# Kernel optimization log

Measured on AMD Instinct MI355X. Metric: run time of the kernel, lower is better.

Reference implementation:

```python
import jax, jax.numpy as jnp
import numpy as np

B, H, W = 16, 352, 352
EPS = 1e-7

# Directable[TL_table[i]] for i = 0..7: (dx, dy), dx=+1 shifts right, dy=+1 shifts down
# TL_table = [lower_right, down, lower_left, right, left, upper_right, up, upper_left]
SHIFTS = [(1, 1), (0, 1), (-1, 1), (1, 0), (-1, 0), (1, -1), (0, -1), (-1, -1)]


def _shift(x, dx, dy):
    # x: [B,H,W]; zero-padded translation, equivalent to the bmm against the
    # near-identity translation matrices in the original code.
    if dx == 1:
        x = jnp.pad(x, ((0, 0), (0, 0), (1, 0)))[:, :, :-1]
    elif dx == -1:
        x = jnp.pad(x, ((0, 0), (0, 0), (0, 1)))[:, :, 1:]
    if dy == 1:
        x = jnp.pad(x, ((0, 0), (1, 0), (0, 0)))[:, :-1, :]
    elif dy == -1:
        x = jnp.pad(x, ((0, 0), (0, 1), (0, 0)))[:, 1:, :]
    return x


def _bce_sum(p, t):
    p = jnp.clip(p, EPS, 1.0 - EPS)
    return -jnp.sum(t * jnp.log(p) + (1.0 - t) * jnp.log1p(-p))


def setup_inputs() -> dict:
    key = jax.random.key(0)
    k1, k2, k3 = jax.random.split(key, 3)
    c_map = jax.random.normal(k1, (B, 8, H, W), dtype=jnp.float32)
    target = jax.random.uniform(k2, (B, 1, H, W), dtype=jnp.float32)
    con_target = jax.random.randint(k3, (B, 8, H, W), 0, 2, dtype=jnp.int32)
    return {"c_map": c_map, "target": target, "con_target": con_target}


def reference(c_map, target, con_target):
    p = jax.nn.sigmoid(c_map)                      # [B,8,H,W]
    con = con_target.astype(p.dtype)
    sum_conn = jnp.sum(con, axis=1)                # [B,H,W]
    edge = ((sum_conn < 8) & (sum_conn > 0)).astype(p.dtype)

    # Bilateral voting: shifted[:, i] = shift(p[:, 7-i], direction_i)
    shifted = jnp.stack(
        [_shift(p[:, 7 - i], *SHIFTS[i]) for i in range(8)], axis=1
    )                                              # [B,8,H,W]
    vote = p * shifted                             # [B,8,H,W]

    glo_map = jnp.max(vote, axis=1)                # [B,H,W]
    pred_mask_min = jnp.min(vote, axis=1)          # [B,H,W]
    decouple = glo_map * (1.0 - edge) + (1.0 - pred_mask_min) * edge

    de_loss = _bce_sum(decouple[:, None], target)
    conmap_l = _bce_sum(p, con)
    bimap_l = _bce_sum(vote, con)
    return 0.8 * conmap_l + de_loss + 0.2 * bimap_l
```

## Files before the change

kernel.cpp:

```cpp
#include <hip/hip_runtime.h>


#define EPSF 1e-7f

constexpr int B = 16, H = 352, W = 352;
constexpr int HW = H * W;
constexpr int N = B * HW;
constexpr int W4 = W / 4;
constexpr int HW4 = HW / 4;
constexpr int NQ = N / 4;
constexpr int NBLK = NQ / 256;

typedef float f4 __attribute__((ext_vector_type(4)));
typedef int   i4 __attribute__((ext_vector_type(4)));

__device__ __forceinline__ float rcpf(float x) { return __builtin_amdgcn_rcpf(x); }

__device__ __forceinline__ f4 sigmoid4(f4 x) {
    f4 r;
    r.x = rcpf(1.0f + __expf(-x.x));
    r.y = rcpf(1.0f + __expf(-x.y));
    r.z = rcpf(1.0f + __expf(-x.z));
    r.w = rcpf(1.0f + __expf(-x.w));
    return r;
}
__device__ __forceinline__ f4 max4(f4 a, f4 b) {
    f4 r; r.x=fmaxf(a.x,b.x); r.y=fmaxf(a.y,b.y); r.z=fmaxf(a.z,b.z); r.w=fmaxf(a.w,b.w); return r;
}
__device__ __forceinline__ f4 min4(f4 a, f4 b) {
    f4 r; r.x=fminf(a.x,b.x); r.y=fminf(a.y,b.y); r.z=fminf(a.z,b.z); r.w=fminf(a.w,b.w); return r;
}
__device__ __forceinline__ f4 sel4(i4 q, f4 a, f4 b) {
    f4 r; r.x=q.x?a.x:b.x; r.y=q.y?a.y:b.y; r.z=q.z?a.z:b.z; r.w=q.w?a.w:b.w; return r;
}
__device__ __forceinline__ f4 loadu4(const float* p) {
    f4 v; __builtin_memcpy(&v, p, sizeof(f4)); return v;
}

__device__ __forceinline__ float finish_pixel(float glo, float pmin, int sc,
                                              float t, float cp, float ba, float bb) {
    const float edge = (sc < 8 && sc > 0) ? 1.0f : 0.0f;
    float dec = glo * (1.0f - edge) + (1.0f - pmin) * edge;
    dec = fminf(fmaxf(dec, EPSF), 1.0f - EPSF);
    const float de = -(t * __logf(dec) + (1.0f - t) * __logf(1.0f - dec));
    return de - 0.8f * __logf(cp) - 0.2f * (__logf(ba) + __logf(bb));
}

__global__ __launch_bounds__(256, 4) void bicon_loss_kernel(
    const float* __restrict__ c_map,
    const float* __restrict__ target,
    const int*   __restrict__ con,
    float* __restrict__ ws)
{
    const int tid = blockIdx.x * blockDim.x + threadIdx.x;
    const int b  = tid / HW4;
    const int rq = tid - b * HW4;
    const int y  = rq / W4;
    const int xq = rq - y * W4;
    const int x0 = xq * 4;

    const float* __restrict__ cm = c_map + (size_t)b * 8 * HW + y * W + x0;
    const int*   __restrict__ cn = con   + (size_t)b * 8 * HW + y * W + x0;

    const f4 c0 = *(const f4*)(cm + 0 * HW);
    const f4 c1 = *(const f4*)(cm + 1 * HW);
    const f4 c2 = *(const f4*)(cm + 2 * HW);
    const f4 c3 = *(const f4*)(cm + 3 * HW);
    const f4 c4 = *(const f4*)(cm + 4 * HW);
    const f4 c5 = *(const f4*)(cm + 5 * HW);
    const f4 c6 = *(const f4*)(cm + 6 * HW);
    const f4 c7 = *(const f4*)(cm + 7 * HW);
    const f4 n0 = loadu4(cm + 7 * HW - 1 * W - 1);
    const f4 n1 = *(const f4*)(cm + 6 * HW - 1 * W);
    const f4 n2 = loadu4(cm + 5 * HW - 1 * W + 1);
    const f4 n3 = loadu4(cm + 4 * HW - 1);
    const f4 n4 = loadu4(cm + 3 * HW + 1);
    const f4 n5 = loadu4(cm + 2 * HW + 1 * W - 1);
    const f4 n6 = *(const f4*)(cm + 1 * HW + 1 * W);
    const f4 n7 = loadu4(cm + 0 * HW + 1 * W + 1);
    const i4 q0 = *(const i4*)(cn + 0 * HW);
    const i4 q1 = *(const i4*)(cn + 1 * HW);
    const i4 q2 = *(const i4*)(cn + 2 * HW);
    const i4 q3 = *(const i4*)(cn + 3 * HW);
    const i4 q4 = *(const i4*)(cn + 4 * HW);
    const i4 q5 = *(const i4*)(cn + 5 * HW);
    const i4 q6 = *(const i4*)(cn + 6 * HW);
    const i4 q7 = *(const i4*)(cn + 7 * HW);
    const f4 t4 = *(const f4*)(target + (size_t)b * HW + y * W + x0);

    const f4 p0 = sigmoid4(c0);
    const f4 p1 = sigmoid4(c1);
    const f4 p2 = sigmoid4(c2);
    const f4 p3 = sigmoid4(c3);
    const f4 p4 = sigmoid4(c4);
    const f4 p5 = sigmoid4(c5);
    const f4 p6 = sigmoid4(c6);
    const f4 p7 = sigmoid4(c7);

    const float lm = (xq == 0)      ? 0.0f : 1.0f;
    const float rm = (xq == W4 - 1) ? 0.0f : 1.0f;
    const float tm = (y == 0)       ? 0.0f : 1.0f;
    const float bm = (y == H - 1)   ? 0.0f : 1.0f;

    f4 conprod = {1.f,1.f,1.f,1.f};
    f4 biA     = {1.f,1.f,1.f,1.f};
    f4 biB     = {1.f,1.f,1.f,1.f};
    f4 glo     = {-1e30f,-1e30f,-1e30f,-1e30f};
    f4 pmin    = { 1e30f, 1e30f, 1e30f, 1e30f};

#define DIR(P, Q, NR, DX, RMASK, BI) {                                        \
        f4 s = sigmoid4(NR);                                                  \
        s *= (RMASK);                                                         \
        if ((DX) == 1)  s.x *= lm;                                            \
        if ((DX) == -1) s.w *= rm;                                            \
        const f4 v = (P) * s;                                                 \
        glo  = max4(glo,  v);                                                 \
        pmin = min4(pmin, v);                                                 \
        conprod *= sel4((Q), (P), 1.0f - (P));                                \
        BI *= sel4((Q), max4(v, (f4){EPSF,EPSF,EPSF,EPSF}), 1.0f - v);        \
    }
    DIR(p0, q0, n0,  1, tm, biA)
    DIR(p1, q1, n1,  0, tm, biA)
    DIR(p2, q2, n2, -1, tm, biA)
    DIR(p3, q3, n3,  1, 1.0f, biA)
    DIR(p4, q4, n4, -1, 1.0f, biB)
    DIR(p5, q5, n5,  1, bm, biB)
    DIR(p6, q6, n6,  0, bm, biB)
    DIR(p7, q7, n7, -1, bm, biB)
#undef DIR

    const i4 sc = q0 + q1 + q2 + q3 + q4 + q5 + q6 + q7;

    float part = finish_pixel(glo.x, pmin.x, sc.x, t4.x, conprod.x, biA.x, biB.x)
               + finish_pixel(glo.y, pmin.y, sc.y, t4.y, conprod.y, biA.y, biB.y)
               + finish_pixel(glo.z, pmin.z, sc.z, t4.z, conprod.z, biA.z, biB.z)
               + finish_pixel(glo.w, pmin.w, sc.w, t4.w, conprod.w, biA.w, biB.w);

    #pragma unroll
    for (int off = 32; off > 0; off >>= 1)
        part += __shfl_down(part, off, 64);

    __shared__ float wsum[4];
    const int lane = threadIdx.x & 63;
    const int wid  = threadIdx.x >> 6;
    if (lane == 0) wsum[wid] = part;
    __syncthreads();
    if (threadIdx.x == 0) {
        ws[blockIdx.x] = wsum[0] + wsum[1] + wsum[2] + wsum[3];
    }
}

__global__ __launch_bounds__(256) void reduce_partials_kernel(
    const float* __restrict__ ws, float* __restrict__ out)
{
    float s = 0.0f;
    for (int i = threadIdx.x; i < NBLK; i += 256) s += ws[i];
    #pragma unroll
    for (int off = 32; off > 0; off >>= 1)
        s += __shfl_down(s, off, 64);
    __shared__ float wsum[4];
    const int lane = threadIdx.x & 63;
    const int wid  = threadIdx.x >> 6;
    if (lane == 0) wsum[wid] = s;
    __syncthreads();
    if (threadIdx.x == 0) out[0] = wsum[0] + wsum[1] + wsum[2] + wsum[3];
}

extern "C" void kernel_launch(void* const* d_in, const int* in_sizes, int n_in,
                              void* d_out, int out_size, void* d_ws, size_t ws_size,
                              hipStream_t stream) {
    const float* c_map  = (const float*)d_in[0];
    const float* target = (const float*)d_in[1];
    const int*   con    = (const int*)d_in[2];
    float* out = (float*)d_out;
    float* ws  = (float*)d_ws;

    bicon_loss_kernel<<<NBLK, 256, 0, stream>>>(c_map, target, con, ws);
    reduce_partials_kernel<<<1, 256, 0, stream>>>(ws, out);
}
```

Measured before the change: 150.4 us.

## Process two rows per thread, reuse vertical neighbor sigmoids, remap blocks across XCDs

Each thread now handles a 4x2 pixel tile instead of 4x1. Row A's up-neighbor for direction 6 and row B's down-neighbor for direction 1 are the same sigmoid values already computed for the other row, so two loads and two sigmoids per tile are reused. Block indices are also remapped so that consecutive logical blocks land on the same XCD, which is meant to improve L2 locality for the halo loads. The trade-off is half as many threads and higher register pressure per thread.

```diff
diff --git a/kernel.cpp b/kernel.cpp
--- a/kernel.cpp
+++ b/kernel.cpp
@@ -7,9 +7,10 @@
 constexpr int HW = H * W;
 constexpr int N = B * HW;
 constexpr int W4 = W / 4;
-constexpr int HW4 = HW / 4;
-constexpr int NQ = N / 4;
-constexpr int NBLK = NQ / 256;
+constexpr int HW8 = HW / 8;
+constexpr int NT = N / 8;
+constexpr int NBLK = NT / 256;
+constexpr int PER_XCD = NBLK / 8;
 
 typedef float f4 __attribute__((ext_vector_type(4)));
 typedef int   i4 __attribute__((ext_vector_type(4)));
@@ -46,70 +47,8 @@
     return de - 0.8f * __logf(cp) - 0.2f * (__logf(ba) + __logf(bb));
 }
 
-__global__ __launch_bounds__(256, 4) void bicon_loss_kernel(
-    const float* __restrict__ c_map,
-    const float* __restrict__ target,
-    const int*   __restrict__ con,
-    float* __restrict__ ws)
-{
-    const int tid = blockIdx.x * blockDim.x + threadIdx.x;
-    const int b  = tid / HW4;
-    const int rq = tid - b * HW4;
-    const int y  = rq / W4;
-    const int xq = rq - y * W4;
-    const int x0 = xq * 4;
-
-    const float* __restrict__ cm = c_map + (size_t)b * 8 * HW + y * W + x0;
-    const int*   __restrict__ cn = con   + (size_t)b * 8 * HW + y * W + x0;
-
-    const f4 c0 = *(const f4*)(cm + 0 * HW);
-    const f4 c1 = *(const f4*)(cm + 1 * HW);
-    const f4 c2 = *(const f4*)(cm + 2 * HW);
-    const f4 c3 = *(const f4*)(cm + 3 * HW);
-    const f4 c4 = *(const f4*)(cm + 4 * HW);
-    const f4 c5 = *(const f4*)(cm + 5 * HW);
-    const f4 c6 = *(const f4*)(cm + 6 * HW);
-    const f4 c7 = *(const f4*)(cm + 7 * HW);
-    const f4 n0 = loadu4(cm + 7 * HW - 1 * W - 1);
-    const f4 n1 = *(const f4*)(cm + 6 * HW - 1 * W);
-    const f4 n2 = loadu4(cm + 5 * HW - 1 * W + 1);
-    const f4 n3 = loadu4(cm + 4 * HW - 1);
-    const f4 n4 = loadu4(cm + 3 * HW + 1);
-    const f4 n5 = loadu4(cm + 2 * HW + 1 * W - 1);
-    const f4 n6 = *(const f4*)(cm + 1 * HW + 1 * W);
-    const f4 n7 = loadu4(cm + 0 * HW + 1 * W + 1);
-    const i4 q0 = *(const i4*)(cn + 0 * HW);
-    const i4 q1 = *(const i4*)(cn + 1 * HW);
-    const i4 q2 = *(const i4*)(cn + 2 * HW);
-    const i4 q3 = *(const i4*)(cn + 3 * HW);
-    const i4 q4 = *(const i4*)(cn + 4 * HW);
-    const i4 q5 = *(const i4*)(cn + 5 * HW);
-    const i4 q6 = *(const i4*)(cn + 6 * HW);
-    const i4 q7 = *(const i4*)(cn + 7 * HW);
-    const f4 t4 = *(const f4*)(target + (size_t)b * HW + y * W + x0);
-
-    const f4 p0 = sigmoid4(c0);
-    const f4 p1 = sigmoid4(c1);
-    const f4 p2 = sigmoid4(c2);
-    const f4 p3 = sigmoid4(c3);
-    const f4 p4 = sigmoid4(c4);
-    const f4 p5 = sigmoid4(c5);
-    const f4 p6 = sigmoid4(c6);
-    const f4 p7 = sigmoid4(c7);
-
-    const float lm = (xq == 0)      ? 0.0f : 1.0f;
-    const float rm = (xq == W4 - 1) ? 0.0f : 1.0f;
-    const float tm = (y == 0)       ? 0.0f : 1.0f;
-    const float bm = (y == H - 1)   ? 0.0f : 1.0f;
-
-    f4 conprod = {1.f,1.f,1.f,1.f};
-    f4 biA     = {1.f,1.f,1.f,1.f};
-    f4 biB     = {1.f,1.f,1.f,1.f};
-    f4 glo     = {-1e30f,-1e30f,-1e30f,-1e30f};
-    f4 pmin    = { 1e30f, 1e30f, 1e30f, 1e30f};
-
-#define DIR(P, Q, NR, DX, RMASK, BI) {                                        \
-        f4 s = sigmoid4(NR);                                                  \
+#define DIRS(P, Q, S, DX, RMASK, BI) {                                        \
+        f4 s = (S);                                                           \
         s *= (RMASK);                                                         \
         if ((DX) == 1)  s.x *= lm;                                            \
         if ((DX) == -1) s.w *= rm;                                            \
@@ -119,22 +58,143 @@
         conprod *= sel4((Q), (P), 1.0f - (P));                                \
         BI *= sel4((Q), max4(v, (f4){EPSF,EPSF,EPSF,EPSF}), 1.0f - v);        \
     }
-    DIR(p0, q0, n0,  1, tm, biA)
-    DIR(p1, q1, n1,  0, tm, biA)
-    DIR(p2, q2, n2, -1, tm, biA)
-    DIR(p3, q3, n3,  1, 1.0f, biA)
-    DIR(p4, q4, n4, -1, 1.0f, biB)
-    DIR(p5, q5, n5,  1, bm, biB)
-    DIR(p6, q6, n6,  0, bm, biB)
-    DIR(p7, q7, n7, -1, bm, biB)
-#undef DIR
-
-    const i4 sc = q0 + q1 + q2 + q3 + q4 + q5 + q6 + q7;
-
-    float part = finish_pixel(glo.x, pmin.x, sc.x, t4.x, conprod.x, biA.x, biB.x)
-               + finish_pixel(glo.y, pmin.y, sc.y, t4.y, conprod.y, biA.y, biB.y)
-               + finish_pixel(glo.z, pmin.z, sc.z, t4.z, conprod.z, biA.z, biB.z)
-               + finish_pixel(glo.w, pmin.w, sc.w, t4.w, conprod.w, biA.w, biB.w);
+
+__global__ __launch_bounds__(256, 4) void bicon_loss_kernel(
+    const float* __restrict__ c_map,
+    const float* __restrict__ target,
+    const int*   __restrict__ con,
+    float* __restrict__ ws)
+{
+    const int lb  = (blockIdx.x & 7) * PER_XCD + (blockIdx.x >> 3);
+    const int tid = lb * 256 + threadIdx.x;
+    const int b   = tid / HW8;
+    const int rem = tid - b * HW8;
+    const int rp  = rem / W4;
+    const int xq  = rem - rp * W4;
+    const int y0  = rp * 2;
+    const int x0  = xq * 4;
+
+    const float* __restrict__ cm = c_map + (size_t)b * 8 * HW + y0 * W + x0;
+    const int*   __restrict__ cn = con   + (size_t)b * 8 * HW + y0 * W + x0;
+    const float* __restrict__ tg = target + (size_t)b * HW + y0 * W + x0;
+
+    const float lm  = (xq == 0)      ? 0.0f : 1.0f;
+    const float rm  = (xq == W4 - 1) ? 0.0f : 1.0f;
+    const float tmA = (y0 == 0)      ? 0.0f : 1.0f;
+    const float bmB = (y0 == H - 2)  ? 0.0f : 1.0f;
+
+    const f4 cA0 = *(const f4*)(cm + 0 * HW);
+    const f4 cA1 = *(const f4*)(cm + 1 * HW);
+    const f4 cA2 = *(const f4*)(cm + 2 * HW);
+    const f4 cA3 = *(const f4*)(cm + 3 * HW);
+    const f4 cA4 = *(const f4*)(cm + 4 * HW);
+    const f4 cA5 = *(const f4*)(cm + 5 * HW);
+    const f4 cA6 = *(const f4*)(cm + 6 * HW);
+    const f4 cA7 = *(const f4*)(cm + 7 * HW);
+    const f4 cB1 = *(const f4*)(cm + 1 * HW + W);
+    const f4 nA0 = loadu4(cm + 7 * HW - W - 1);
+    const f4 nA1 = *(const f4*)(cm + 6 * HW - W);
+    const f4 nA2 = loadu4(cm + 5 * HW - W + 1);
+    const f4 nA3 = loadu4(cm + 4 * HW - 1);
+    const f4 nA4 = loadu4(cm + 3 * HW + 1);
+    const f4 nA5 = loadu4(cm + 2 * HW + W - 1);
+    const f4 nA7 = loadu4(cm + 0 * HW + W + 1);
+    const i4 qA0 = *(const i4*)(cn + 0 * HW);
+    const i4 qA1 = *(const i4*)(cn + 1 * HW);
+    const i4 qA2 = *(const i4*)(cn + 2 * HW);
+    const i4 qA3 = *(const i4*)(cn + 3 * HW);
+    const i4 qA4 = *(const i4*)(cn + 4 * HW);
+    const i4 qA5 = *(const i4*)(cn + 5 * HW);
+    const i4 qA6 = *(const i4*)(cn + 6 * HW);
+    const i4 qA7 = *(const i4*)(cn + 7 * HW);
+    const f4 tA  = *(const f4*)(tg);
+
+    const f4 pA0 = sigmoid4(cA0);
+    const f4 pA1 = sigmoid4(cA1);
+    const f4 pA2 = sigmoid4(cA2);
+    const f4 pA3 = sigmoid4(cA3);
+    const f4 pA4 = sigmoid4(cA4);
+    const f4 pA5 = sigmoid4(cA5);
+    const f4 pA6 = sigmoid4(cA6);
+    const f4 pA7 = sigmoid4(cA7);
+    const f4 pB1 = sigmoid4(cB1);
+
+    float part;
+    {
+        f4 conprod = {1.f,1.f,1.f,1.f};
+        f4 biA     = {1.f,1.f,1.f,1.f};
+        f4 biB     = {1.f,1.f,1.f,1.f};
+        f4 glo     = {-1e30f,-1e30f,-1e30f,-1e30f};
+        f4 pmin    = { 1e30f, 1e30f, 1e30f, 1e30f};
+        DIRS(pA0, qA0, sigmoid4(nA0),  1, tmA,  biA)
+        DIRS(pA1, qA1, sigmoid4(nA1),  0, tmA,  biA)
+        DIRS(pA2, qA2, sigmoid4(nA2), -1, tmA,  biA)
+        DIRS(pA3, qA3, sigmoid4(nA3),  1, 1.0f, biA)
+        DIRS(pA4, qA4, sigmoid4(nA4), -1, 1.0f, biB)
+        DIRS(pA5, qA5, sigmoid4(nA5),  1, 1.0f, biB)
+        DIRS(pA6, qA6, pB1,            0, 1.0f, biB)
+        DIRS(pA7, qA7, sigmoid4(nA7), -1, 1.0f, biB)
+        const i4 sc = qA0 + qA1 + qA2 + qA3 + qA4 + qA5 + qA6 + qA7;
+        part = finish_pixel(glo.x, pmin.x, sc.x, tA.x, conprod.x, biA.x, biB.x)
+             + finish_pixel(glo.y, pmin.y, sc.y, tA.y, conprod.y, biA.y, biB.y)
+             + finish_pixel(glo.z, pmin.z, sc.z, tA.z, conprod.z, biA.z, biB.z)
+             + finish_pixel(glo.w, pmin.w, sc.w, tA.w, conprod.w, biA.w, biB.w);
+    }
+
+    const float* cmB = cm + W;
+    const int*   cnB = cn + W;
+    const f4 cB0 = *(const f4*)(cmB + 0 * HW);
+    const f4 cB2 = *(const f4*)(cmB + 2 * HW);
+    const f4 cB3 = *(const f4*)(cmB + 3 * HW);
+    const f4 cB4 = *(const f4*)(cmB + 4 * HW);
+    const f4 cB5 = *(const f4*)(cmB + 5 * HW);
+    const f4 cB6 = *(const f4*)(cmB + 6 * HW);
+    const f4 cB7 = *(const f4*)(cmB + 7 * HW);
+    const f4 nB0 = loadu4(cmB + 7 * HW - W - 1);
+    const f4 nB2 = loadu4(cmB + 5 * HW - W + 1);
+    const f4 nB3 = loadu4(cmB + 4 * HW - 1);
+    const f4 nB4 = loadu4(cmB + 3 * HW + 1);
+    const f4 nB5 = loadu4(cmB + 2 * HW + W - 1);
+    const f4 nB6 = *(const f4*)(cmB + 1 * HW + W);
+    const f4 nB7 = loadu4(cmB + 0 * HW + W + 1);
+    const i4 qB0 = *(const i4*)(cnB + 0 * HW);
+    const i4 qB1 = *(const i4*)(cnB + 1 * HW);
+    const i4 qB2 = *(const i4*)(cnB + 2 * HW);
+    const i4 qB3 = *(const i4*)(cnB + 3 * HW);
+    const i4 qB4 = *(const i4*)(cnB + 4 * HW);
+    const i4 qB5 = *(const i4*)(cnB + 5 * HW);
+    const i4 qB6 = *(const i4*)(cnB + 6 * HW);
+    const i4 qB7 = *(const i4*)(cnB + 7 * HW);
+    const f4 tB  = *(const f4*)(tg + W);
+
+    const f4 pB0 = sigmoid4(cB0);
+    const f4 pB2 = sigmoid4(cB2);
+    const f4 pB3 = sigmoid4(cB3);
+    const f4 pB4 = sigmoid4(cB4);
+    const f4 pB5 = sigmoid4(cB5);
+    const f4 pB6 = sigmoid4(cB6);
+    const f4 pB7 = sigmoid4(cB7);
+
+    {
+        f4 conprod = {1.f,1.f,1.f,1.f};
+        f4 biA     = {1.f,1.f,1.f,1.f};
+        f4 biB     = {1.f,1.f,1.f,1.f};
+        f4 glo     = {-1e30f,-1e30f,-1e30f,-1e30f};
+        f4 pmin    = { 1e30f, 1e30f, 1e30f, 1e30f};
+        DIRS(pB0, qB0, sigmoid4(nB0),  1, 1.0f, biA)
+        DIRS(pB1, qB1, pA6,            0, 1.0f, biA)
+        DIRS(pB2, qB2, sigmoid4(nB2), -1, 1.0f, biA)
+        DIRS(pB3, qB3, sigmoid4(nB3),  1, 1.0f, biA)
+        DIRS(pB4, qB4, sigmoid4(nB4), -1, 1.0f, biB)
+        DIRS(pB5, qB5, sigmoid4(nB5),  1, bmB,  biB)
+        DIRS(pB6, qB6, sigmoid4(nB6),  0, bmB,  biB)
+        DIRS(pB7, qB7, sigmoid4(nB7), -1, bmB,  biB)
+        const i4 sc = qB0 + qB1 + qB2 + qB3 + qB4 + qB5 + qB6 + qB7;
+        part += finish_pixel(glo.x, pmin.x, sc.x, tB.x, conprod.x, biA.x, biB.x)
+              + finish_pixel(glo.y, pmin.y, sc.y, tB.y, conprod.y, biA.y, biB.y)
+              + finish_pixel(glo.z, pmin.z, sc.z, tB.z, conprod.z, biA.z, biB.z)
+              + finish_pixel(glo.w, pmin.w, sc.w, tB.w, conprod.w, biA.w, biB.w);
+    }
 
     #pragma unroll
     for (int off = 32; off > 0; off >>= 1)
```

After: 156.1 us. +3.8%, slower.

## Stage sigmoid tiles with halo in fp16 shared memory to reuse neighbors

Applied to the files above, without the earlier changes.

Each block now handles a tile of 2816 pixels of one batch image. It first loads all 8 channels plus a one-row halo on each side, applies the sigmoid once, and stores the results as fp16 in LDS. The compute phase then reads centre and shifted neighbours from LDS instead of issuing a second set of unaligned global loads and a second sigmoid per direction. This halves the c_map global reads and the exp work. In exchange it adds a block barrier and LDS traffic, loses precision by storing probabilities in fp16 (which affects the log terms), and uses about 53KB of LDS, which limits occupancy.

```diff
diff --git a/kernel.cpp b/kernel.cpp
--- a/kernel.cpp
+++ b/kernel.cpp
@@ -5,14 +5,19 @@
 
 constexpr int B = 16, H = 352, W = 352;
 constexpr int HW = H * W;
-constexpr int N = B * HW;
-constexpr int W4 = W / 4;
-constexpr int HW4 = HW / 4;
-constexpr int NQ = N / 4;
-constexpr int NBLK = NQ / 256;
-
-typedef float f4 __attribute__((ext_vector_type(4)));
-typedef int   i4 __attribute__((ext_vector_type(4)));
+constexpr int TILE_PX = 2816;
+constexpr int TILES = HW / TILE_PX;
+constexpr int NBLK = B * TILES;
+constexpr int TILE_Q = TILE_PX / 4;
+constexpr int HALO = 384;
+constexpr int STAGE_PX = TILE_PX + 2 * HALO;
+constexpr int STAGE_Q  = STAGE_PX / 4;
+constexpr int STAGE_ALL_Q = 8 * STAGE_Q;
+constexpr int SITER = STAGE_ALL_Q / 256;
+
+typedef float    f4 __attribute__((ext_vector_type(4)));
+typedef int      i4 __attribute__((ext_vector_type(4)));
+typedef _Float16 h4 __attribute__((ext_vector_type(4)));
 
 __device__ __forceinline__ float rcpf(float x) { return __builtin_amdgcn_rcpf(x); }
 
@@ -30,11 +35,14 @@
 __device__ __forceinline__ f4 min4(f4 a, f4 b) {
     f4 r; r.x=fminf(a.x,b.x); r.y=fminf(a.y,b.y); r.z=fminf(a.z,b.z); r.w=fminf(a.w,b.w); return r;
 }
-__device__ __forceinline__ f4 sel4(i4 q, f4 a, f4 b) {
-    f4 r; r.x=q.x?a.x:b.x; r.y=q.y?a.y:b.y; r.z=q.z?a.z:b.z; r.w=q.w?a.w:b.w; return r;
-}
-__device__ __forceinline__ f4 loadu4(const float* p) {
-    f4 v; __builtin_memcpy(&v, p, sizeof(f4)); return v;
+__device__ __forceinline__ f4 sel4(i4 m, f4 a, f4 b) {
+    f4 r; r.x=m.x?a.x:b.x; r.y=m.y?a.y:b.y; r.z=m.z?a.z:b.z; r.w=m.w?a.w:b.w; return r;
+}
+__device__ __forceinline__ f4 cvt4(h4 h) {
+    f4 r; r.x=(float)h.x; r.y=(float)h.y; r.z=(float)h.z; r.w=(float)h.w; return r;
+}
+__device__ __forceinline__ f4 rd4(const _Float16* p) {
+    f4 r; r.x=(float)p[0]; r.y=(float)p[1]; r.z=(float)p[2]; r.w=(float)p[3]; return r;
 }
 
 __device__ __forceinline__ float finish_pixel(float glo, float pmin, int sc,
@@ -46,108 +54,125 @@
     return de - 0.8f * __logf(cp) - 0.2f * (__logf(ba) + __logf(bb));
 }
 
-__global__ __launch_bounds__(256, 4) void bicon_loss_kernel(
+__global__ __launch_bounds__(256) void bicon_loss_kernel(
     const float* __restrict__ c_map,
     const float* __restrict__ target,
     const int*   __restrict__ con,
     float* __restrict__ ws)
 {
-    const int tid = blockIdx.x * blockDim.x + threadIdx.x;
-    const int b  = tid / HW4;
-    const int rq = tid - b * HW4;
-    const int y  = rq / W4;
-    const int xq = rq - y * W4;
-    const int x0 = xq * 4;
-
-    const float* __restrict__ cm = c_map + (size_t)b * 8 * HW + y * W + x0;
-    const int*   __restrict__ cn = con   + (size_t)b * 8 * HW + y * W + x0;
-
-    const f4 c0 = *(const f4*)(cm + 0 * HW);
-    const f4 c1 = *(const f4*)(cm + 1 * HW);
-    const f4 c2 = *(const f4*)(cm + 2 * HW);
-    const f4 c3 = *(const f4*)(cm + 3 * HW);
-    const f4 c4 = *(const f4*)(cm + 4 * HW);
-    const f4 c5 = *(const f4*)(cm + 5 * HW);
-    const f4 c6 = *(const f4*)(cm + 6 * HW);
-    const f4 c7 = *(const f4*)(cm + 7 * HW);
-    const f4 n0 = loadu4(cm + 7 * HW - 1 * W - 1);
-    const f4 n1 = *(const f4*)(cm + 6 * HW - 1 * W);
-    const f4 n2 = loadu4(cm + 5 * HW - 1 * W + 1);
-    const f4 n3 = loadu4(cm + 4 * HW - 1);
-    const f4 n4 = loadu4(cm + 3 * HW + 1);
-    const f4 n5 = loadu4(cm + 2 * HW + 1 * W - 1);
-    const f4 n6 = *(const f4*)(cm + 1 * HW + 1 * W);
-    const f4 n7 = loadu4(cm + 0 * HW + 1 * W + 1);
-    const i4 q0 = *(const i4*)(cn + 0 * HW);
-    const i4 q1 = *(const i4*)(cn + 1 * HW);
-    const i4 q2 = *(const i4*)(cn + 2 * HW);
-    const i4 q3 = *(const i4*)(cn + 3 * HW);
-    const i4 q4 = *(const i4*)(cn + 4 * HW);
-    const i4 q5 = *(const i4*)(cn + 5 * HW);
-    const i4 q6 = *(const i4*)(cn + 6 * HW);
-    const i4 q7 = *(const i4*)(cn + 7 * HW);
-    const f4 t4 = *(const f4*)(target + (size_t)b * HW + y * W + x0);
-
-    const f4 p0 = sigmoid4(c0);
-    const f4 p1 = sigmoid4(c1);
-    const f4 p2 = sigmoid4(c2);
-    const f4 p3 = sigmoid4(c3);
-    const f4 p4 = sigmoid4(c4);
-    const f4 p5 = sigmoid4(c5);
-    const f4 p6 = sigmoid4(c6);
-    const f4 p7 = sigmoid4(c7);
-
-    const float lm = (xq == 0)      ? 0.0f : 1.0f;
-    const float rm = (xq == W4 - 1) ? 0.0f : 1.0f;
-    const float tm = (y == 0)       ? 0.0f : 1.0f;
-    const float bm = (y == H - 1)   ? 0.0f : 1.0f;
-
-    f4 conprod = {1.f,1.f,1.f,1.f};
-    f4 biA     = {1.f,1.f,1.f,1.f};
-    f4 biB     = {1.f,1.f,1.f,1.f};
-    f4 glo     = {-1e30f,-1e30f,-1e30f,-1e30f};
-    f4 pmin    = { 1e30f, 1e30f, 1e30f, 1e30f};
-
-#define DIR(P, Q, NR, DX, RMASK, BI) {                                        \
-        f4 s = sigmoid4(NR);                                                  \
-        s *= (RMASK);                                                         \
-        if ((DX) == 1)  s.x *= lm;                                            \
-        if ((DX) == -1) s.w *= rm;                                            \
-        const f4 v = (P) * s;                                                 \
-        glo  = max4(glo,  v);                                                 \
-        pmin = min4(pmin, v);                                                 \
-        conprod *= sel4((Q), (P), 1.0f - (P));                                \
-        BI *= sel4((Q), max4(v, (f4){EPSF,EPSF,EPSF,EPSF}), 1.0f - v);        \
+    __shared__ _Float16 Lh[8 * STAGE_PX];
+    __shared__ float wsum[4];
+
+    const int blk  = blockIdx.x;
+    const int b    = blk / TILES;
+    const int tile = blk - b * TILES;
+    const int s    = tile * TILE_PX;
+    const int s0   = s - HALO;
+
+    const float* __restrict__ cmb = c_map + (size_t)b * 8 * HW;
+    const int*   __restrict__ cnb = con   + (size_t)b * 8 * HW;
+    const float* __restrict__ tgb = target + (size_t)b * HW;
+
+    #pragma unroll
+    for (int k = 0; k < SITER; ++k) {
+        const int q   = threadIdx.x + k * 256;
+        const int ch  = q / STAGE_Q;
+        const int idx = q - ch * STAGE_Q;
+        int px = s0 + idx * 4;
+        px = px < 0 ? 0 : (px > HW - 4 ? HW - 4 : px);
+        const f4 v = *(const f4*)(cmb + ch * HW + px);
+        const f4 p = sigmoid4(v);
+        h4 hp; hp.x=(_Float16)p.x; hp.y=(_Float16)p.y; hp.z=(_Float16)p.z; hp.w=(_Float16)p.w;
+        *(h4*)(&Lh[q * 4]) = hp;
     }
-    DIR(p0, q0, n0,  1, tm, biA)
-    DIR(p1, q1, n1,  0, tm, biA)
-    DIR(p2, q2, n2, -1, tm, biA)
-    DIR(p3, q3, n3,  1, 1.0f, biA)
-    DIR(p4, q4, n4, -1, 1.0f, biB)
-    DIR(p5, q5, n5,  1, bm, biB)
-    DIR(p6, q6, n6,  0, bm, biB)
-    DIR(p7, q7, n7, -1, bm, biB)
+    __syncthreads();
+
+    float part = 0.0f;
+    #pragma unroll
+    for (int k = 0; k < 3; ++k) {
+        const int qi = threadIdx.x + k * 256;
+        if (qi < TILE_Q) {
+            const int gp  = s + qi * 4;
+            const int y   = gp / W;
+            const int xq4 = (gp - y * W) >> 2;
+            const float lm = (xq4 == 0)         ? 0.0f : 1.0f;
+            const float rm = (xq4 == W / 4 - 1) ? 0.0f : 1.0f;
+            const float tm = (y == 0)           ? 0.0f : 1.0f;
+            const float bm = (y == H - 1)       ? 0.0f : 1.0f;
+            const int l0 = qi * 4 + HALO;
+
+            const i4 g0 = *(const i4*)(cnb + 0 * HW + gp);
+            const i4 g1 = *(const i4*)(cnb + 1 * HW + gp);
+            const i4 g2 = *(const i4*)(cnb + 2 * HW + gp);
+            const i4 g3 = *(const i4*)(cnb + 3 * HW + gp);
+            const i4 g4 = *(const i4*)(cnb + 4 * HW + gp);
+            const i4 g5 = *(const i4*)(cnb + 5 * HW + gp);
+            const i4 g6 = *(const i4*)(cnb + 6 * HW + gp);
+            const i4 g7 = *(const i4*)(cnb + 7 * HW + gp);
+            const f4 t4 = *(const f4*)(tgb + gp);
+
+            const f4 p0 = cvt4(*(const h4*)&Lh[0 * STAGE_PX + l0]);
+            const f4 p1 = cvt4(*(const h4*)&Lh[1 * STAGE_PX + l0]);
+            const f4 p2 = cvt4(*(const h4*)&Lh[2 * STAGE_PX + l0]);
+            const f4 p3 = cvt4(*(const h4*)&Lh[3 * STAGE_PX + l0]);
+            const f4 p4 = cvt4(*(const h4*)&Lh[4 * STAGE_PX + l0]);
+            const f4 p5 = cvt4(*(const h4*)&Lh[5 * STAGE_PX + l0]);
+            const f4 p6 = cvt4(*(const h4*)&Lh[6 * STAGE_PX + l0]);
+            const f4 p7 = cvt4(*(const h4*)&Lh[7 * STAGE_PX + l0]);
+            const f4 n0 = rd4(&Lh[7 * STAGE_PX + l0 - W - 1]);
+            const f4 n1 = cvt4(*(const h4*)&Lh[6 * STAGE_PX + l0 - W]);
+            const f4 n2 = rd4(&Lh[5 * STAGE_PX + l0 - W + 1]);
+            const f4 n3 = rd4(&Lh[4 * STAGE_PX + l0 - 1]);
+            const f4 n4 = rd4(&Lh[3 * STAGE_PX + l0 + 1]);
+            const f4 n5 = rd4(&Lh[2 * STAGE_PX + l0 + W - 1]);
+            const f4 n6 = cvt4(*(const h4*)&Lh[1 * STAGE_PX + l0 + W]);
+            const f4 n7 = rd4(&Lh[0 * STAGE_PX + l0 + W + 1]);
+
+            f4 conprod = {1.f,1.f,1.f,1.f};
+            f4 biA     = {1.f,1.f,1.f,1.f};
+            f4 biB     = {1.f,1.f,1.f,1.f};
+            f4 glo     = {-1e30f,-1e30f,-1e30f,-1e30f};
+            f4 pmin    = { 1e30f, 1e30f, 1e30f, 1e30f};
+
+#define DIR(P, G, S, DX, RMASK, BI) {                                         \
+            f4 sv = (S);                                                      \
+            sv *= (RMASK);                                                    \
+            if ((DX) == 1)  sv.x *= lm;                                       \
+            if ((DX) == -1) sv.w *= rm;                                       \
+            const f4 v = (P) * sv;                                            \
+            glo  = max4(glo,  v);                                             \
+            pmin = min4(pmin, v);                                             \
+            conprod *= sel4((G), (P), 1.0f - (P));                            \
+            BI *= sel4((G), max4(v, (f4){EPSF,EPSF,EPSF,EPSF}), 1.0f - v);    \
+        }
+            DIR(p0, g0, n0,  1, tm,   biA)
+            DIR(p1, g1, n1,  0, tm,   biA)
+            DIR(p2, g2, n2, -1, tm,   biA)
+            DIR(p3, g3, n3,  1, 1.0f, biA)
+            DIR(p4, g4, n4, -1, 1.0f, biB)
+            DIR(p5, g5, n5,  1, bm,   biB)
+            DIR(p6, g6, n6,  0, bm,   biB)
+            DIR(p7, g7, n7, -1, bm,   biB)
 #undef DIR
 
-    const i4 sc = q0 + q1 + q2 + q3 + q4 + q5 + q6 + q7;
-
-    float part = finish_pixel(glo.x, pmin.x, sc.x, t4.x, conprod.x, biA.x, biB.x)
-               + finish_pixel(glo.y, pmin.y, sc.y, t4.y, conprod.y, biA.y, biB.y)
-               + finish_pixel(glo.z, pmin.z, sc.z, t4.z, conprod.z, biA.z, biB.z)
-               + finish_pixel(glo.w, pmin.w, sc.w, t4.w, conprod.w, biA.w, biB.w);
+            const i4 sc = g0 + g1 + g2 + g3 + g4 + g5 + g6 + g7;
+            part += finish_pixel(glo.x, pmin.x, sc.x, t4.x, conprod.x, biA.x, biB.x)
+                  + finish_pixel(glo.y, pmin.y, sc.y, t4.y, conprod.y, biA.y, biB.y)
+                  + finish_pixel(glo.z, pmin.z, sc.z, t4.z, conprod.z, biA.z, biB.z)
+                  + finish_pixel(glo.w, pmin.w, sc.w, t4.w, conprod.w, biA.w, biB.w);
+        }
+    }
 
     #pragma unroll
     for (int off = 32; off > 0; off >>= 1)
         part += __shfl_down(part, off, 64);
 
-    __shared__ float wsum[4];
     const int lane = threadIdx.x & 63;
     const int wid  = threadIdx.x >> 6;
     if (lane == 0) wsum[wid] = part;
     __syncthreads();
-    if (threadIdx.x == 0) {
+    if (threadIdx.x == 0)
         ws[blockIdx.x] = wsum[0] + wsum[1] + wsum[2] + wsum[3];
-    }
 }
 
 __global__ __launch_bounds__(256) void reduce_partials_kernel(
```

Measured after the change: 150.7 us. About the same (+0.2%).
